# Performance work log

Hardware: AMD Instinct MI355X
Metric: run time of the kernel (lower is better)

The kernel has to match this reference:

```python
import jax, jax.numpy as jnp
import numpy as np

ALPHA = 1.0
BETA = 1.0
B, C, F = 16384, 2000, 1024

def setup_inputs() -> dict:
    key = jax.random.key(0)
    k1, k2, k3, k4 = jax.random.split(key, 4)
    features = jax.random.normal(k1, (B, F), dtype=jnp.float32)
    labels = jax.random.randint(k2, (B,), 0, C, dtype=jnp.int64)
    centers = jax.random.normal(k3, (C, F), dtype=jnp.float32)
    W = jax.random.normal(k4, (C, F), dtype=jnp.float32) * (1.0 / np.sqrt(F))
    b = jnp.zeros((C,), dtype=jnp.float32)
    return {"features": features, "labels": labels, "centers": centers, "W": W, "b": b}

def reference(features, labels, centers, W, b):
    # Fisher (center) loss: only the true-class center distance is used, so
    # gather centers[labels] instead of materializing the [B, C, F] broadcast.
    diff = features - centers[labels]                     # [B, F]
    fisher_loss = jnp.mean(jnp.sum(diff * diff, axis=1))  # scalar
    # Aux cross-entropy over a linear classifier.
    logits = jnp.einsum('bf,cf->bc', features, W) + b     # [B, C]
    logZ = jax.nn.logsumexp(logits, axis=1)               # [B]
    true_logit = jnp.take_along_axis(logits, labels[:, None], axis=1)[:, 0]
    aux_loss = jnp.mean(logZ - true_logit)
    return ALPHA * fisher_loss + BETA * aux_loss
```

## Files before the change

### kernel.cpp

```cpp
#include <hip/hip_runtime.h>
#include <stdint.h>

#define B_ROWS 16384
#define C_CLS  2000
#define C_PAD  2048
#define F_DIM  1024
#define KT     16
#define NRB    128
#define NCBP   16
#define PANEL_B 131072

typedef float f32x4 __attribute__((ext_vector_type(4)));
typedef long long i64x2 __attribute__((ext_vector_type(2)));

#define SCALE_F 4.0f
#define SCALE_W 16.0f
#define INV_SCALE 0.015625f

__device__ __forceinline__ unsigned int pk4(float a, float b, float c, float d) {
    int u = __builtin_amdgcn_cvt_pk_fp8_f32(a, b, 0, false);
    u = __builtin_amdgcn_cvt_pk_fp8_f32(c, d, u, true);
    return (unsigned int)u;
}


__global__ __launch_bounds__(256)
void prepA_kernel(const float* __restrict__ feat, const int* __restrict__ labels,
                  const float* __restrict__ centers,
                  char* __restrict__ A_pre, float* __restrict__ fisher_part)
{
    const int rt = blockIdx.x >> 2, g = blockIdx.x & 3;
    const int tid = threadIdx.x;
    const int r = tid >> 1, h = tid & 1;
    const int grow = rt * 128 + r;
    const int lab = labels[grow];
    const float* frow = feat    + (size_t)grow * F_DIM;
    const float* crow = centers + (size_t)lab  * F_DIM;
    char* pan = A_pre + (size_t)rt * PANEL_B + (r >> 4) * 1024 + (r & 15) * 16;
    float facc = 0.f;
    #pragma unroll
    for (int q = 0; q < 4; ++q) {
        const int kt = g * 4 + q;
        #pragma unroll
        for (int u = 0; u < 2; ++u) {
            const int lhi = h * 2 + u;
            const int k0 = kt * 64 + lhi * 8;
            float4 a0 = *(const float4*)(frow + k0);
            float4 a1 = *(const float4*)(frow + k0 + 4);
            float4 a2 = *(const float4*)(frow + k0 + 32);
            float4 a3 = *(const float4*)(frow + k0 + 36);
            float4 c0 = *(const float4*)(crow + k0);
            float4 c1 = *(const float4*)(crow + k0 + 4);
            float4 c2 = *(const float4*)(crow + k0 + 32);
            float4 c3 = *(const float4*)(crow + k0 + 36);
            float d0 = a0.x-c0.x, d1 = a0.y-c0.y, d2 = a0.z-c0.z, d3 = a0.w-c0.w;
            float d4 = a1.x-c1.x, d5 = a1.y-c1.y, d6 = a1.z-c1.z, d7 = a1.w-c1.w;
            facc += d0*d0 + d1*d1 + d2*d2 + d3*d3 + d4*d4 + d5*d5 + d6*d6 + d7*d7;
            d0 = a2.x-c2.x; d1 = a2.y-c2.y; d2 = a2.z-c2.z; d3 = a2.w-c2.w;
            d4 = a3.x-c3.x; d5 = a3.y-c3.y; d6 = a3.z-c3.z; d7 = a3.w-c3.w;
            facc += d0*d0 + d1*d1 + d2*d2 + d3*d3 + d4*d4 + d5*d5 + d6*d6 + d7*d7;
            uint4 o = { pk4(SCALE_F*a0.x, SCALE_F*a0.y, SCALE_F*a0.z, SCALE_F*a0.w),
                        pk4(SCALE_F*a1.x, SCALE_F*a1.y, SCALE_F*a1.z, SCALE_F*a1.w),
                        pk4(SCALE_F*a2.x, SCALE_F*a2.y, SCALE_F*a2.z, SCALE_F*a2.w),
                        pk4(SCALE_F*a3.x, SCALE_F*a3.y, SCALE_F*a3.z, SCALE_F*a3.w) };
            *(uint4*)(pan + kt * 8192 + lhi * 256) = o;
        }
    }
    for (int d = 32; d >= 1; d >>= 1) facc += __shfl_xor(facc, d);
    __shared__ float redw[4];
    const int wid = tid >> 6, lane = tid & 63;
    if (lane == 0) redw[wid] = facc;
    __syncthreads();
    if (tid == 0) fisher_part[blockIdx.x] = redw[0] + redw[1] + redw[2] + redw[3];
}

__global__ __launch_bounds__(256)
void prepB_kernel(const float* __restrict__ W, const float* __restrict__ bias,
                  char* __restrict__ B_pre, float* __restrict__ bias_pad)
{
    const int ct = blockIdx.x >> 3, ktg = blockIdx.x & 7;
    const int tid = threadIdx.x;
    const int rcol = tid >> 1, h = tid & 1;
    const int gc = ct * 128 + rcol;
    char* pan = B_pre + (size_t)ct * PANEL_B + (rcol >> 4) * 1024 + (rcol & 15) * 16;
    #pragma unroll
    for (int q = 0; q < 2; ++q) {
        const int kt = ktg * 2 + q;
        #pragma unroll
        for (int u = 0; u < 2; ++u) {
            const int lhi = h * 2 + u;
            uint4 o;
            if (gc < C_CLS) {
                const float* src = W + (size_t)gc * F_DIM + kt * 64 + lhi * 8;
                float4 a0 = *(const float4*)(src);
                float4 a1 = *(const float4*)(src + 4);
                float4 a2 = *(const float4*)(src + 32);
                float4 a3 = *(const float4*)(src + 36);
                o = (uint4){ pk4(SCALE_W*a0.x, SCALE_W*a0.y, SCALE_W*a0.z, SCALE_W*a0.w),
                             pk4(SCALE_W*a1.x, SCALE_W*a1.y, SCALE_W*a1.z, SCALE_W*a1.w),
                             pk4(SCALE_W*a2.x, SCALE_W*a2.y, SCALE_W*a2.z, SCALE_W*a2.w),
                             pk4(SCALE_W*a3.x, SCALE_W*a3.y, SCALE_W*a3.z, SCALE_W*a3.w) };
            } else {
                o = (uint4){0u, 0u, 0u, 0u};
            }
            *(uint4*)(pan + kt * 8192 + lhi * 256) = o;
        }
    }
    if (blockIdx.x < C_PAD / 256) {
        const int i = blockIdx.x * 256 + tid;
        bias_pad[i] = (i < C_CLS) ? bias[i] : -1e30f;
    }
}

__global__ __launch_bounds__(256, 3)
void gemm_kernel(const int* __restrict__ labels, const float* __restrict__ biasp,
                 const char* __restrict__ A_pre, const char* __restrict__ B_pre,
                 float* __restrict__ s_part, float* __restrict__ tl_part)
{
    __shared__ float red2[128][2][2];

    const int cpx = gridDim.x >> 3;
    const int wg = (blockIdx.x & 7) * cpx + (blockIdx.x >> 3);
    const int cbp = wg & 15;
    const int rb  = wg >> 4;

    const int tid = threadIdx.x;
    const int w = tid >> 6, lane = tid & 63;
    const int l15 = lane & 15, lhi = lane >> 4;
    const int wr = w >> 1, wcl = w & 1;

    const char* Apan = A_pre + (size_t)rb  * PANEL_B + wr  * 4096 + lane * 16;
    const char* Bpan = B_pre + (size_t)cbp * PANEL_B + wcl * 4096 + lane * 16;

    f32x4 acc[4][4];
    #pragma unroll
    for (int mi = 0; mi < 4; ++mi)
        #pragma unroll
        for (int ni = 0; ni < 4; ++ni) acc[mi][ni] = (f32x4){0.f, 0.f, 0.f, 0.f};

    i64x2 aE[4], bE[4], aO[4], bO[4];

#define LOADT(SA, SB, KTT) do {                                                       \
    const char* pa_ = Apan + (KTT) * 8192;                                            \
    const char* pb_ = Bpan + (KTT) * 8192;                                            \
    _Pragma("unroll")                                                                 \
    for (int i_ = 0; i_ < 4; ++i_) SA[i_] = *(const i64x2*)(pa_ + i_ * 1024);         \
    _Pragma("unroll")                                                                 \
    for (int i_ = 0; i_ < 4; ++i_) SB[i_] = *(const i64x2*)(pb_ + i_ * 1024);         \
} while (0)

#define MFMA32(SA, SB) do {                                                           \
    __builtin_amdgcn_s_setprio(1);                                                    \
    _Pragma("unroll")                                                                 \
    for (int kf_ = 0; kf_ < 2; ++kf_)                                                 \
        _Pragma("unroll")                                                             \
        for (int mi_ = 0; mi_ < 4; ++mi_)                                             \
            _Pragma("unroll")                                                         \
            for (int ni_ = 0; ni_ < 4; ++ni_)                                         \
                acc[mi_][ni_] = __builtin_amdgcn_mfma_f32_16x16x32_fp8_fp8(           \
                    SA[mi_][kf_], SB[ni_][kf_], acc[mi_][ni_], 0, 0, 0);              \
    __builtin_amdgcn_s_setprio(0);                                                    \
} while (0)

#define FENCE __builtin_amdgcn_sched_barrier(0)

    LOADT(aE, bE, 0);
    FENCE;
    #pragma unroll 1
    for (int k2 = 0; k2 < 7; ++k2) {
        LOADT(aO, bO, 2 * k2 + 1);
        FENCE;
        MFMA32(aE, bE);
        FENCE;
        LOADT(aE, bE, 2 * k2 + 2);
        FENCE;
        MFMA32(aO, bO);
        FENCE;
    }
    LOADT(aO, bO, 15);
    FENCE;
    MFMA32(aE, bE);
    MFMA32(aO, bO);

#undef LOADT
#undef MFMA32
#undef FENCE

    float bb[4];
    #pragma unroll
    for (int ni = 0; ni < 4; ++ni)
        bb[ni] = biasp[cbp * 128 + wcl * 64 + ni * 16 + l15];

    #pragma unroll
    for (int mi = 0; mi < 4; ++mi) {
        #pragma unroll
        for (int j = 0; j < 4; ++j) {
            const int rl = wr * 64 + mi * 16 + lhi * 4 + j;
            const int lab = labels[rb * 128 + rl];
            float sv = 0.f, tv = 0.f;
            #pragma unroll
            for (int ni = 0; ni < 4; ++ni) {
                const float v = fmaf(acc[mi][ni][j], INV_SCALE, bb[ni]);
                sv += __expf(v);
                const int gc = cbp * 128 + wcl * 64 + ni * 16 + l15;
                tv = (gc == lab) ? v : tv;
            }
            #pragma unroll
            for (int d = 1; d < 16; d <<= 1) {
                sv += __shfl_xor(sv, d);
                tv += __shfl_xor(tv, d);
            }
            if (l15 == 0) { red2[rl][wcl][0] = sv; red2[rl][wcl][1] = tv; }
        }
    }
    __syncthreads();
    if (tid < 128) {
        const float sv = red2[tid][0][0] + red2[tid][1][0];
        const float tv = red2[tid][0][1] + red2[tid][1][1];
        const int grow = rb * 128 + tid;
        s_part[(size_t)cbp * B_ROWS + grow]  = sv;
        tl_part[(size_t)cbp * B_ROWS + grow] = tv;
    }
}

__global__ __launch_bounds__(256)
void rowcomb_kernel(const float* __restrict__ s_part, const float* __restrict__ tl_part,
                    float* __restrict__ aux_part)
{
    const int row = blockIdx.x * 256 + threadIdx.x;
    float s = 0.f, t = 0.f;
    #pragma unroll
    for (int p = 0; p < NCBP; ++p) {
        s += s_part[(size_t)p * B_ROWS + row];
        t += tl_part[(size_t)p * B_ROWS + row];
    }
    float acc = __logf(s) - t;
    for (int d = 32; d >= 1; d >>= 1) acc += __shfl_xor(acc, d);
    __shared__ float red[4];
    const int wid = threadIdx.x >> 6, lane = threadIdx.x & 63;
    if (lane == 0) red[wid] = acc;
    __syncthreads();
    if (threadIdx.x == 0) aux_part[blockIdx.x] = red[0] + red[1] + red[2] + red[3];
}

__global__ __launch_bounds__(256)
void final_kernel(const float* __restrict__ fisher_part, const float* __restrict__ aux_part,
                  float* __restrict__ out)
{
    const int tid = threadIdx.x;
    float acc = fisher_part[tid] + fisher_part[256 + tid];
    if (tid < 64) acc += aux_part[tid];
    for (int d = 32; d >= 1; d >>= 1) acc += __shfl_xor(acc, d);
    __shared__ float red[4];
    const int wid = tid >> 6, lane = tid & 63;
    if (lane == 0) red[wid] = acc;
    __syncthreads();
    if (tid == 0) out[0] = (red[0] + red[1] + red[2] + red[3]) * (1.0f / (float)B_ROWS);
}

extern "C" void kernel_launch(void* const* d_in, const int* in_sizes, int n_in,
                              void* d_out, int out_size, void* d_ws, size_t ws_size,
                              hipStream_t stream)
{
    (void)in_sizes; (void)n_in; (void)out_size; (void)ws_size;
    const float* feat    = (const float*)d_in[0];
    const int*   labels  = (const int*)  d_in[1];
    const float* centers = (const float*)d_in[2];
    const float* W       = (const float*)d_in[3];
    const float* bias    = (const float*)d_in[4];
    float* out = (float*)d_out;
    char* ws = (char*)d_ws;

    const size_t szA    = (size_t)NRB  * PANEL_B;
    const size_t szB    = (size_t)NCBP * PANEL_B;
    const size_t szBias = (size_t)C_PAD * 4;

    char* A_pre = ws;
    char* B_pre = ws + szA;
    float* bias_pad    = (float*)(ws + szA + szB);
    float* s_part      = (float*)(ws + szA + szB + szBias);
    float* tl_part     = s_part + (size_t)NCBP * B_ROWS;
    float* fisher_part = tl_part + (size_t)NCBP * B_ROWS;
    float* aux_part    = fisher_part + 512;

    prepA_kernel<<<512, 256, 0, stream>>>(feat, labels, centers, A_pre, fisher_part);
    prepB_kernel<<<128, 256, 0, stream>>>(W, bias, B_pre, bias_pad);
    gemm_kernel<<<NRB * NCBP, 256, 0, stream>>>(labels, bias_pad, A_pre, B_pre, s_part, tl_part);
    rowcomb_kernel<<<B_ROWS / 256, 256, 0, stream>>>(s_part, tl_part, aux_part);
    final_kernel<<<1, 256, 0, stream>>>(fisher_part, aux_part, out);
}
```

Before: 86.84 us.

## Enlarge GEMM tile to 256x128 rows per block and merge prep kernels

Doubles the row tile so each block covers 256 rows and 128 classes, with each wave computing a 64x128 subtile (4x8 MFMA accumulators). The A panels are re-laid out to 256-row panels, and the cross-wave LDS reduction is dropped because each wave now spans all 128 columns and writes partials directly. The two prep kernels are fused into one launch to save a kernel launch. More accumulator registers lower occupancy (launch bounds go from 3 to 2 blocks per CU) and halve the grid size, in exchange for fewer B reloads and more MFMA work per load.

```diff
diff --git a/kernel.cpp b/kernel.cpp
--- a/kernel.cpp
+++ b/kernel.cpp
@@ -6,9 +6,10 @@
 #define C_PAD  2048
 #define F_DIM  1024
 #define KT     16
-#define NRB    128
+#define NRB    64
 #define NCBP   16
-#define PANEL_B 131072
+#define PANEL_A 262144
+#define PANEL_BB 131072
 
 typedef float f32x4 __attribute__((ext_vector_type(4)));
 typedef long long i64x2 __attribute__((ext_vector_type(2)));
@@ -25,138 +26,136 @@
 
 
 __global__ __launch_bounds__(256)
-void prepA_kernel(const float* __restrict__ feat, const int* __restrict__ labels,
-                  const float* __restrict__ centers,
-                  char* __restrict__ A_pre, float* __restrict__ fisher_part)
-{
-    const int rt = blockIdx.x >> 2, g = blockIdx.x & 3;
+void prep_kernel(const float* __restrict__ feat, const int* __restrict__ labels,
+                 const float* __restrict__ centers, const float* __restrict__ W,
+                 const float* __restrict__ bias,
+                 char* __restrict__ A_pre, char* __restrict__ B_pre,
+                 float* __restrict__ bias_pad, float* __restrict__ fisher_part)
+{
     const int tid = threadIdx.x;
-    const int r = tid >> 1, h = tid & 1;
-    const int grow = rt * 128 + r;
-    const int lab = labels[grow];
-    const float* frow = feat    + (size_t)grow * F_DIM;
-    const float* crow = centers + (size_t)lab  * F_DIM;
-    char* pan = A_pre + (size_t)rt * PANEL_B + (r >> 4) * 1024 + (r & 15) * 16;
-    float facc = 0.f;
-    #pragma unroll
-    for (int q = 0; q < 4; ++q) {
-        const int kt = g * 4 + q;
-        #pragma unroll
-        for (int u = 0; u < 2; ++u) {
-            const int lhi = h * 2 + u;
-            const int k0 = kt * 64 + lhi * 8;
-            float4 a0 = *(const float4*)(frow + k0);
-            float4 a1 = *(const float4*)(frow + k0 + 4);
-            float4 a2 = *(const float4*)(frow + k0 + 32);
-            float4 a3 = *(const float4*)(frow + k0 + 36);
-            float4 c0 = *(const float4*)(crow + k0);
-            float4 c1 = *(const float4*)(crow + k0 + 4);
-            float4 c2 = *(const float4*)(crow + k0 + 32);
-            float4 c3 = *(const float4*)(crow + k0 + 36);
-            float d0 = a0.x-c0.x, d1 = a0.y-c0.y, d2 = a0.z-c0.z, d3 = a0.w-c0.w;
-            float d4 = a1.x-c1.x, d5 = a1.y-c1.y, d6 = a1.z-c1.z, d7 = a1.w-c1.w;
-            facc += d0*d0 + d1*d1 + d2*d2 + d3*d3 + d4*d4 + d5*d5 + d6*d6 + d7*d7;
-            d0 = a2.x-c2.x; d1 = a2.y-c2.y; d2 = a2.z-c2.z; d3 = a2.w-c2.w;
-            d4 = a3.x-c3.x; d5 = a3.y-c3.y; d6 = a3.z-c3.z; d7 = a3.w-c3.w;
-            facc += d0*d0 + d1*d1 + d2*d2 + d3*d3 + d4*d4 + d5*d5 + d6*d6 + d7*d7;
-            uint4 o = { pk4(SCALE_F*a0.x, SCALE_F*a0.y, SCALE_F*a0.z, SCALE_F*a0.w),
-                        pk4(SCALE_F*a1.x, SCALE_F*a1.y, SCALE_F*a1.z, SCALE_F*a1.w),
-                        pk4(SCALE_F*a2.x, SCALE_F*a2.y, SCALE_F*a2.z, SCALE_F*a2.w),
-                        pk4(SCALE_F*a3.x, SCALE_F*a3.y, SCALE_F*a3.z, SCALE_F*a3.w) };
-            *(uint4*)(pan + kt * 8192 + lhi * 256) = o;
-        }
-    }
-    for (int d = 32; d >= 1; d >>= 1) facc += __shfl_xor(facc, d);
-    __shared__ float redw[4];
-    const int wid = tid >> 6, lane = tid & 63;
-    if (lane == 0) redw[wid] = facc;
-    __syncthreads();
-    if (tid == 0) fisher_part[blockIdx.x] = redw[0] + redw[1] + redw[2] + redw[3];
-}
-
-__global__ __launch_bounds__(256)
-void prepB_kernel(const float* __restrict__ W, const float* __restrict__ bias,
-                  char* __restrict__ B_pre, float* __restrict__ bias_pad)
-{
-    const int ct = blockIdx.x >> 3, ktg = blockIdx.x & 7;
-    const int tid = threadIdx.x;
-    const int rcol = tid >> 1, h = tid & 1;
-    const int gc = ct * 128 + rcol;
-    char* pan = B_pre + (size_t)ct * PANEL_B + (rcol >> 4) * 1024 + (rcol & 15) * 16;
-    #pragma unroll
-    for (int q = 0; q < 2; ++q) {
-        const int kt = ktg * 2 + q;
-        #pragma unroll
-        for (int u = 0; u < 2; ++u) {
-            const int lhi = h * 2 + u;
-            uint4 o;
-            if (gc < C_CLS) {
-                const float* src = W + (size_t)gc * F_DIM + kt * 64 + lhi * 8;
-                float4 a0 = *(const float4*)(src);
-                float4 a1 = *(const float4*)(src + 4);
-                float4 a2 = *(const float4*)(src + 32);
-                float4 a3 = *(const float4*)(src + 36);
-                o = (uint4){ pk4(SCALE_W*a0.x, SCALE_W*a0.y, SCALE_W*a0.z, SCALE_W*a0.w),
-                             pk4(SCALE_W*a1.x, SCALE_W*a1.y, SCALE_W*a1.z, SCALE_W*a1.w),
-                             pk4(SCALE_W*a2.x, SCALE_W*a2.y, SCALE_W*a2.z, SCALE_W*a2.w),
-                             pk4(SCALE_W*a3.x, SCALE_W*a3.y, SCALE_W*a3.z, SCALE_W*a3.w) };
-            } else {
-                o = (uint4){0u, 0u, 0u, 0u};
-            }
-            *(uint4*)(pan + kt * 8192 + lhi * 256) = o;
-        }
-    }
-    if (blockIdx.x < C_PAD / 256) {
-        const int i = blockIdx.x * 256 + tid;
-        bias_pad[i] = (i < C_CLS) ? bias[i] : -1e30f;
-    }
-}
-
-__global__ __launch_bounds__(256, 3)
+    if (blockIdx.x < 512) {
+        const int rt = blockIdx.x >> 2, g = blockIdx.x & 3;
+        const int rb = rt >> 1;
+        const int r = tid >> 1, h = tid & 1;
+        const int grow = rt * 128 + r;
+        const int lab = labels[grow];
+        const float* frow = feat    + (size_t)grow * F_DIM;
+        const float* crow = centers + (size_t)lab  * F_DIM;
+        const int frag = (rt & 1) * 8 + (r >> 4);
+        char* pan = A_pre + (size_t)rb * PANEL_A + frag * 1024 + (r & 15) * 16;
+        float facc = 0.f;
+        #pragma unroll
+        for (int q = 0; q < 4; ++q) {
+            const int kt = g * 4 + q;
+            #pragma unroll
+            for (int u = 0; u < 2; ++u) {
+                const int lhi = h * 2 + u;
+                const int k0 = kt * 64 + lhi * 8;
+                float4 a0 = *(const float4*)(frow + k0);
+                float4 a1 = *(const float4*)(frow + k0 + 4);
+                float4 a2 = *(const float4*)(frow + k0 + 32);
+                float4 a3 = *(const float4*)(frow + k0 + 36);
+                float4 c0 = *(const float4*)(crow + k0);
+                float4 c1 = *(const float4*)(crow + k0 + 4);
+                float4 c2 = *(const float4*)(crow + k0 + 32);
+                float4 c3 = *(const float4*)(crow + k0 + 36);
+                float d0 = a0.x-c0.x, d1 = a0.y-c0.y, d2 = a0.z-c0.z, d3 = a0.w-c0.w;
+                float d4 = a1.x-c1.x, d5 = a1.y-c1.y, d6 = a1.z-c1.z, d7 = a1.w-c1.w;
+                facc += d0*d0 + d1*d1 + d2*d2 + d3*d3 + d4*d4 + d5*d5 + d6*d6 + d7*d7;
+                d0 = a2.x-c2.x; d1 = a2.y-c2.y; d2 = a2.z-c2.z; d3 = a2.w-c2.w;
+                d4 = a3.x-c3.x; d5 = a3.y-c3.y; d6 = a3.z-c3.z; d7 = a3.w-c3.w;
+                facc += d0*d0 + d1*d1 + d2*d2 + d3*d3 + d4*d4 + d5*d5 + d6*d6 + d7*d7;
+                uint4 o = { pk4(SCALE_F*a0.x, SCALE_F*a0.y, SCALE_F*a0.z, SCALE_F*a0.w),
+                            pk4(SCALE_F*a1.x, SCALE_F*a1.y, SCALE_F*a1.z, SCALE_F*a1.w),
+                            pk4(SCALE_F*a2.x, SCALE_F*a2.y, SCALE_F*a2.z, SCALE_F*a2.w),
+                            pk4(SCALE_F*a3.x, SCALE_F*a3.y, SCALE_F*a3.z, SCALE_F*a3.w) };
+                *(uint4*)(pan + kt * 16384 + lhi * 256) = o;
+            }
+        }
+        for (int d = 32; d >= 1; d >>= 1) facc += __shfl_xor(facc, d);
+        __shared__ float redw[4];
+        const int wid = tid >> 6, lane = tid & 63;
+        if (lane == 0) redw[wid] = facc;
+        __syncthreads();
+        if (tid == 0) fisher_part[blockIdx.x] = redw[0] + redw[1] + redw[2] + redw[3];
+    } else {
+        const int b = blockIdx.x - 512;
+        const int ct = b >> 3, ktg = b & 7;
+        const int rcol = tid >> 1, h = tid & 1;
+        const int gc = ct * 128 + rcol;
+        char* pan = B_pre + (size_t)ct * PANEL_BB + (rcol >> 4) * 1024 + (rcol & 15) * 16;
+        #pragma unroll
+        for (int q = 0; q < 2; ++q) {
+            const int kt = ktg * 2 + q;
+            #pragma unroll
+            for (int u = 0; u < 2; ++u) {
+                const int lhi = h * 2 + u;
+                uint4 o;
+                if (gc < C_CLS) {
+                    const float* src = W + (size_t)gc * F_DIM + kt * 64 + lhi * 8;
+                    float4 a0 = *(const float4*)(src);
+                    float4 a1 = *(const float4*)(src + 4);
+                    float4 a2 = *(const float4*)(src + 32);
+                    float4 a3 = *(const float4*)(src + 36);
+                    o = (uint4){ pk4(SCALE_W*a0.x, SCALE_W*a0.y, SCALE_W*a0.z, SCALE_W*a0.w),
+                                 pk4(SCALE_W*a1.x, SCALE_W*a1.y, SCALE_W*a1.z, SCALE_W*a1.w),
+                                 pk4(SCALE_W*a2.x, SCALE_W*a2.y, SCALE_W*a2.z, SCALE_W*a2.w),
+                                 pk4(SCALE_W*a3.x, SCALE_W*a3.y, SCALE_W*a3.z, SCALE_W*a3.w) };
+                } else {
+                    o = (uint4){0u, 0u, 0u, 0u};
+                }
+                *(uint4*)(pan + kt * 8192 + lhi * 256) = o;
+            }
+        }
+        if (b < C_PAD / 256) {
+            const int i = b * 256 + tid;
+            bias_pad[i] = (i < C_CLS) ? bias[i] : -1e30f;
+        }
+    }
+}
+
+__global__ __launch_bounds__(256, 2)
 void gemm_kernel(const int* __restrict__ labels, const float* __restrict__ biasp,
                  const char* __restrict__ A_pre, const char* __restrict__ B_pre,
                  float* __restrict__ s_part, float* __restrict__ tl_part)
 {
-    __shared__ float red2[128][2][2];
-
     const int cpx = gridDim.x >> 3;
     const int wg = (blockIdx.x & 7) * cpx + (blockIdx.x >> 3);
-    const int cbp = wg & 15;
-    const int rb  = wg >> 4;
+    const int cb = wg & 15;
+    const int rb = wg >> 4;
 
     const int tid = threadIdx.x;
     const int w = tid >> 6, lane = tid & 63;
     const int l15 = lane & 15, lhi = lane >> 4;
-    const int wr = w >> 1, wcl = w & 1;
-
-    const char* Apan = A_pre + (size_t)rb  * PANEL_B + wr  * 4096 + lane * 16;
-    const char* Bpan = B_pre + (size_t)cbp * PANEL_B + wcl * 4096 + lane * 16;
-
-    f32x4 acc[4][4];
+
+    const char* Apan = A_pre + (size_t)rb * PANEL_A + w * 4096 + lane * 16;
+    const char* Bpan = B_pre + (size_t)cb * PANEL_BB + lane * 16;
+
+    f32x4 acc[4][8];
     #pragma unroll
     for (int mi = 0; mi < 4; ++mi)
         #pragma unroll
-        for (int ni = 0; ni < 4; ++ni) acc[mi][ni] = (f32x4){0.f, 0.f, 0.f, 0.f};
-
-    i64x2 aE[4], bE[4], aO[4], bO[4];
+        for (int ni = 0; ni < 8; ++ni) acc[mi][ni] = (f32x4){0.f, 0.f, 0.f, 0.f};
+
+    i64x2 aE[4], bE[8], aO[4], bO[8];
 
 #define LOADT(SA, SB, KTT) do {                                                       \
-    const char* pa_ = Apan + (KTT) * 8192;                                            \
+    const char* pa_ = Apan + (KTT) * 16384;                                           \
     const char* pb_ = Bpan + (KTT) * 8192;                                            \
     _Pragma("unroll")                                                                 \
     for (int i_ = 0; i_ < 4; ++i_) SA[i_] = *(const i64x2*)(pa_ + i_ * 1024);         \
     _Pragma("unroll")                                                                 \
-    for (int i_ = 0; i_ < 4; ++i_) SB[i_] = *(const i64x2*)(pb_ + i_ * 1024);         \
+    for (int i_ = 0; i_ < 8; ++i_) SB[i_] = *(const i64x2*)(pb_ + i_ * 1024);         \
 } while (0)
 
-#define MFMA32(SA, SB) do {                                                           \
+#define MFMA64(SA, SB) do {                                                           \
     __builtin_amdgcn_s_setprio(1);                                                    \
     _Pragma("unroll")                                                                 \
     for (int kf_ = 0; kf_ < 2; ++kf_)                                                 \
         _Pragma("unroll")                                                             \
         for (int mi_ = 0; mi_ < 4; ++mi_)                                             \
             _Pragma("unroll")                                                         \
-            for (int ni_ = 0; ni_ < 4; ++ni_)                                         \
+            for (int ni_ = 0; ni_ < 8; ++ni_)                                         \
                 acc[mi_][ni_] = __builtin_amdgcn_mfma_f32_16x16x32_fp8_fp8(           \
                     SA[mi_][kf_], SB[ni_][kf_], acc[mi_][ni_], 0, 0, 0);              \
     __builtin_amdgcn_s_setprio(0);                                                    \
@@ -170,39 +169,39 @@
     for (int k2 = 0; k2 < 7; ++k2) {
         LOADT(aO, bO, 2 * k2 + 1);
         FENCE;
-        MFMA32(aE, bE);
+        MFMA64(aE, bE);
         FENCE;
         LOADT(aE, bE, 2 * k2 + 2);
         FENCE;
-        MFMA32(aO, bO);
+        MFMA64(aO, bO);
         FENCE;
     }
     LOADT(aO, bO, 15);
     FENCE;
-    MFMA32(aE, bE);
-    MFMA32(aO, bO);
+    MFMA64(aE, bE);
+    MFMA64(aO, bO);
 
 #undef LOADT
-#undef MFMA32
+#undef MFMA64
 #undef FENCE
 
-    float bb[4];
-    #pragma unroll
-    for (int ni = 0; ni < 4; ++ni)
-        bb[ni] = biasp[cbp * 128 + wcl * 64 + ni * 16 + l15];
+    float bb[8];
+    #pragma unroll
+    for (int ni = 0; ni < 8; ++ni)
+        bb[ni] = biasp[cb * 128 + ni * 16 + l15];
 
     #pragma unroll
     for (int mi = 0; mi < 4; ++mi) {
         #pragma unroll
         for (int j = 0; j < 4; ++j) {
-            const int rl = wr * 64 + mi * 16 + lhi * 4 + j;
-            const int lab = labels[rb * 128 + rl];
+            const int rl = w * 64 + mi * 16 + lhi * 4 + j;
+            const int lab = labels[rb * 256 + rl];
             float sv = 0.f, tv = 0.f;
             #pragma unroll
-            for (int ni = 0; ni < 4; ++ni) {
+            for (int ni = 0; ni < 8; ++ni) {
                 const float v = fmaf(acc[mi][ni][j], INV_SCALE, bb[ni]);
                 sv += __expf(v);
-                const int gc = cbp * 128 + wcl * 64 + ni * 16 + l15;
+                const int gc = cb * 128 + ni * 16 + l15;
                 tv = (gc == lab) ? v : tv;
             }
             #pragma unroll
@@ -210,16 +209,12 @@
                 sv += __shfl_xor(sv, d);
                 tv += __shfl_xor(tv, d);
             }
-            if (l15 == 0) { red2[rl][wcl][0] = sv; red2[rl][wcl][1] = tv; }
-        }
-    }
-    __syncthreads();
-    if (tid < 128) {
-        const float sv = red2[tid][0][0] + red2[tid][1][0];
-        const float tv = red2[tid][0][1] + red2[tid][1][1];
-        const int grow = rb * 128 + tid;
-        s_part[(size_t)cbp * B_ROWS + grow]  = sv;
-        tl_part[(size_t)cbp * B_ROWS + grow] = tv;
+            if (l15 == 0) {
+                const int grow = rb * 256 + rl;
+                s_part[(size_t)cb * B_ROWS + grow]  = sv;
+                tl_part[(size_t)cb * B_ROWS + grow] = tv;
+            }
+        }
     }
 }
 
@@ -271,8 +266,8 @@
     float* out = (float*)d_out;
     char* ws = (char*)d_ws;
 
-    const size_t szA    = (size_t)NRB  * PANEL_B;
-    const size_t szB    = (size_t)NCBP * PANEL_B;
+    const size_t szA    = (size_t)NRB  * PANEL_A;
+    const size_t szB    = (size_t)NCBP * PANEL_BB;
     const size_t szBias = (size_t)C_PAD * 4;
 
     char* A_pre = ws;
@@ -283,8 +278,8 @@
     float* fisher_part = tl_part + (size_t)NCBP * B_ROWS;
     float* aux_part    = fisher_part + 512;
 
-    prepA_kernel<<<512, 256, 0, stream>>>(feat, labels, centers, A_pre, fisher_part);
-    prepB_kernel<<<128, 256, 0, stream>>>(W, bias, B_pre, bias_pad);
+    prep_kernel<<<640, 256, 0, stream>>>(feat, labels, centers, W, bias,
+                                         A_pre, B_pre, bias_pad, fisher_part);
     gemm_kernel<<<NRB * NCBP, 256, 0, stream>>>(labels, bias_pad, A_pre, B_pre, s_part, tl_part);
     rowcomb_kernel<<<B_ROWS / 256, 256, 0, stream>>>(s_part, tl_part, aux_part);
     final_kernel<<<1, 256, 0, stream>>>(fisher_part, aux_part, out);
```

After: 80.66 us. -7.1%, faster.
